# Kernel optimization log

Measured on AMD Instinct MI355X. Metric: run time of the kernel, lower is better.

Reference implementation:

```python
import jax, jax.numpy as jnp
import numpy as np

TOKENS = 16384
HIDDEN = 2048
GROUP_SIZE = 128
EPS = 1e-05
FP8_MAX = 448.0  # float8_e4m3fn max


def rmsnorm(x, w, eps=EPS):
    # vLLM RMSNorm: x * rsqrt(mean(x^2)) * weight
    var = jnp.mean(x * x, axis=-1, keepdims=True)
    return x * jax.lax.rsqrt(var + eps) * w


def fused_add_rmsnorm(x, residual, w, eps=EPS):
    # vLLM RMSNorm(x, residual): residual += x; out = rmsnorm(residual)
    resid = x + residual
    return rmsnorm(resid, w, eps), resid


def per_token_group_quant_fp8_ue8m0(y, group_size=GROUP_SIZE):
    # QuantFP8(static=False, group_shape=(1,128), use_ue8m0=True)
    t, h = y.shape
    g = y.reshape(t, h // group_size, group_size)
    amax = jnp.max(jnp.abs(g), axis=-1)                      # [T, H/G]
    scale = jnp.maximum(amax, 1e-10) / FP8_MAX
    scale = jnp.exp2(jnp.ceil(jnp.log2(scale)))              # ue8m0: round scale up to power of 2
    q = jnp.clip(g / scale[..., None], -FP8_MAX, FP8_MAX)
    q = q.astype(jnp.float8_e4m3fn)                          # fp8 rounding
    return q.reshape(t, h), scale


def setup_inputs() -> dict:
    key = jax.random.key(0)
    kx, kw = jax.random.split(key)
    x = jax.random.normal(kx, (TOKENS, HIDDEN), dtype=jnp.float32)
    norm_w = jnp.ones((4, HIDDEN), dtype=jnp.float32)
    w = jax.random.uniform(kw, (3, HIDDEN, HIDDEN), dtype=jnp.float32)
    return {"x": x, "norm_w": norm_w, "w": w}


def reference(x, norm_w, w):
    # tensor_model_parallel_all_reduce == identity at world_size 1
    z = jax.nn.relu(x)
    xr = z
    resid = z
    y = rmsnorm(xr, norm_w[0])
    x2 = y @ w[0]
    y2, resid = fused_add_rmsnorm(x2, resid, norm_w[1])
    y2_q, y2_s = per_token_group_quant_fp8_ue8m0(y2)
    x3 = y2_q.astype(x.dtype) @ w[1]
    y3, resid = fused_add_rmsnorm(x3, resid, norm_w[2])
    y3_q, y3_s = per_token_group_quant_fp8_ue8m0(y3)
    x4 = y3_q.astype(x.dtype) @ w[2]
    y4, resid = fused_add_rmsnorm(x4, resid, norm_w[3])
    return (y4, y2_s, y3_s)
```

## Files before the change

kernel.cpp:

```cpp
#include <hip/hip_runtime.h>
#include <stdint.h>
#include <math.h>

#define NTOK 16384
#define HID  2048
#define NGRP 16
#define EPSF 1e-5f

typedef __bf16 bf16;
typedef __bf16 bf16x8 __attribute__((ext_vector_type(8)));
typedef float  f32x4  __attribute__((ext_vector_type(4)));


__device__ __forceinline__ void async_load16(const void* g, void* l) {
  __builtin_amdgcn_global_load_lds((const __attribute__((address_space(1))) void*)g,
                                   (__attribute__((address_space(3))) void*)l, 16, 0, 0);
}

__device__ __forceinline__ float fp8_e4m3_rne(float v) {
  float a = fabsf(v);
  float s = (v < 0.f) ? -1.f : 1.f;
  if (a < 0.015625f) {
    float r = rintf(a * 512.0f);
    return s * r * 0.001953125f;
  }
  uint32_t u = __float_as_uint(a);
  u = (u + 0x7FFFFu + ((u >> 20) & 1u)) & 0xFFF00000u;
  return s * __uint_as_float(u);
}

__device__ __forceinline__ float block_sum256(float v) {
  __shared__ float sh[4];
  #pragma unroll
  for (int o = 32; o > 0; o >>= 1) v += __shfl_xor(v, o, 64);
  if ((threadIdx.x & 63) == 0) sh[threadIdx.x >> 6] = v;
  __syncthreads();
  return sh[0] + sh[1] + sh[2] + sh[3];
}

__device__ __forceinline__ float ue8m0_scale(float amax) {
  float v = fmaxf(amax, 1e-10f) / 448.0f;
  float l = (float)log2((double)v);
  return exp2f(ceilf(l));
}


__global__ __launch_bounds__(256) void k_transpose_cast(const float* __restrict__ W,
                                                        bf16* __restrict__ Wt) {
  __shared__ float tile[64][65];
  const size_t mat = (size_t)HID * HID;
  const float* Wz = W + mat * blockIdx.z;
  bf16* Wtz = Wt + mat * blockIdx.z;
  int bn = blockIdx.x * 64;
  int bk = blockIdx.y * 64;
  int t = threadIdx.x;
  {
    int r = t >> 4, c = (t & 15) * 4;
    #pragma unroll
    for (int i = 0; i < 4; i++) {
      float4 v = *(const float4*)(Wz + (size_t)(bk + r + 16 * i) * HID + bn + c);
      tile[r + 16 * i][c] = v.x; tile[r + 16 * i][c + 1] = v.y;
      tile[r + 16 * i][c + 2] = v.z; tile[r + 16 * i][c + 3] = v.w;
    }
  }
  __syncthreads();
  {
    int n = t >> 2, kc = (t & 3) * 16;
    bf16x8 o0, o1;
    #pragma unroll
    for (int j = 0; j < 8; j++) o0[j] = (bf16)tile[kc + j][n];
    #pragma unroll
    for (int j = 0; j < 8; j++) o1[j] = (bf16)tile[kc + 8 + j][n];
    bf16* dst = Wtz + (size_t)(bn + n) * HID + bk + kc;
    *(bf16x8*)dst = o0;
    *(bf16x8*)(dst + 8) = o1;
  }
}

__global__ __launch_bounds__(256) void k_pre(const float* __restrict__ x,
                                             const float* __restrict__ nw,
                                             bf16* __restrict__ Y,
                                             bf16* __restrict__ R) {
  size_t base = (size_t)blockIdx.x * HID + threadIdx.x * 8;
  float4 v0 = *(const float4*)(x + base);
  float4 v1 = *(const float4*)(x + base + 4);
  float z[8] = {v0.x, v0.y, v0.z, v0.w, v1.x, v1.y, v1.z, v1.w};
  float ss = 0.f;
  #pragma unroll
  for (int i = 0; i < 8; i++) { z[i] = fmaxf(z[i], 0.f); ss += z[i] * z[i]; }
  float tot = block_sum256(ss);
  float s = rsqrtf(tot * (1.0f / HID) + EPSF);
  bf16x8 rr;
  #pragma unroll
  for (int i = 0; i < 8; i++) rr[i] = (bf16)z[i];
  *(bf16x8*)(R + base) = rr;
  int j0 = threadIdx.x * 8;
  float4 w0 = *(const float4*)(nw + j0);
  float4 w1 = *(const float4*)(nw + j0 + 4);
  float wv[8] = {w0.x, w0.y, w0.z, w0.w, w1.x, w1.y, w1.z, w1.w};
  bf16x8 o;
  #pragma unroll
  for (int i = 0; i < 8; i++) o[i] = (bf16)(z[i] * s * wv[i]);
  *(bf16x8*)(Y + base) = o;
}

__global__ __launch_bounds__(256) void k_fuse_quant(const bf16* __restrict__ residIn,
                                                    const bf16* __restrict__ Cin,
                                                    const float* __restrict__ nw,
                                                    bf16* __restrict__ residOut,
                                                    bf16* __restrict__ Aout,
                                                    float* __restrict__ scaleOut) {
  int row = blockIdx.x;
  int j0 = threadIdx.x * 8;
  size_t base = (size_t)row * HID + j0;
  bf16x8 c  = *(const bf16x8*)(Cin + base);
  bf16x8 rv = *(const bf16x8*)(residIn + base);
  float r[8]; float ss = 0.f;
  #pragma unroll
  for (int i = 0; i < 8; i++) { r[i] = (float)rv[i] + (float)c[i]; ss += r[i] * r[i]; }
  float tot = block_sum256(ss);
  float s = rsqrtf(tot * (1.0f / HID) + EPSF);

  bf16x8 ro;
  #pragma unroll
  for (int i = 0; i < 8; i++) ro[i] = (bf16)r[i];
  *(bf16x8*)(residOut + base) = ro;

  float4 w0 = *(const float4*)(nw + j0);
  float4 w1 = *(const float4*)(nw + j0 + 4);
  float wv[8] = {w0.x, w0.y, w0.z, w0.w, w1.x, w1.y, w1.z, w1.w};
  float y[8], amax = 0.f;
  #pragma unroll
  for (int i = 0; i < 8; i++) { y[i] = r[i] * s * wv[i]; amax = fmaxf(amax, fabsf(y[i])); }
  amax = fmaxf(amax, __shfl_xor(amax, 1, 64));
  amax = fmaxf(amax, __shfl_xor(amax, 2, 64));
  amax = fmaxf(amax, __shfl_xor(amax, 4, 64));
  amax = fmaxf(amax, __shfl_xor(amax, 8, 64));
  float scale = ue8m0_scale(amax);
  float inv = 1.0f / scale;
  bf16x8 q;
  #pragma unroll
  for (int i = 0; i < 8; i++) {
    float t = fminf(fmaxf(y[i] * inv, -448.f), 448.f);
    q[i] = (bf16)fp8_e4m3_rne(t);
  }
  *(bf16x8*)(Aout + base) = q;
  if ((threadIdx.x & 15) == 0) scaleOut[(size_t)row * NGRP + (j0 >> 7)] = scale;
}

__global__ __launch_bounds__(256) void k_final(const bf16* __restrict__ residIn,
                                               const bf16* __restrict__ Cin,
                                               const float* __restrict__ nw,
                                               float* __restrict__ out) {
  size_t base = (size_t)blockIdx.x * HID + threadIdx.x * 8;
  bf16x8 c  = *(const bf16x8*)(Cin + base);
  bf16x8 rv = *(const bf16x8*)(residIn + base);
  float r[8]; float ss = 0.f;
  #pragma unroll
  for (int i = 0; i < 8; i++) { r[i] = (float)rv[i] + (float)c[i]; ss += r[i] * r[i]; }
  float tot = block_sum256(ss);
  float s = rsqrtf(tot * (1.0f / HID) + EPSF);
  int j0 = threadIdx.x * 8;
  float4 w0 = *(const float4*)(nw + j0);
  float4 w1 = *(const float4*)(nw + j0 + 4);
  float wv[8] = {w0.x, w0.y, w0.z, w0.w, w1.x, w1.y, w1.z, w1.w};
  float4 o0, o1;
  o0.x = r[0]*s*wv[0]; o0.y = r[1]*s*wv[1]; o0.z = r[2]*s*wv[2]; o0.w = r[3]*s*wv[3];
  o1.x = r[4]*s*wv[4]; o1.y = r[5]*s*wv[5]; o1.z = r[6]*s*wv[6]; o1.w = r[7]*s*wv[7];
  *(float4*)(out + base) = o0;
  *(float4*)(out + base + 4) = o1;
}

__global__ __launch_bounds__(512, 2) void k_gemm(const bf16* __restrict__ A,
                                                 const bf16* __restrict__ B,
                                                 bf16* __restrict__ C,
                                                 int M, int N, int K) {
  __shared__ __align__(16) char lds[2 * 65536];
  int b = blockIdx.x;
  int x = b & 7, j = b >> 3;
  int bm = x * 8 + (j & 7);
  int bn = j >> 3;
  int tid = threadIdx.x;
  int wave = tid >> 6, lane = tid & 63;
  int q = lane >> 4, rr = lane & 15;
  int wm = wave >> 2, wn = wave & 3;

  const bf16* aS[2][2]; const bf16* bS[2][2];
  #pragma unroll
  for (int ic = 0; ic < 2; ic++) {
    int m = ic * 512 + tid;
    int lr = m >> 3, cl = m & 7, lc = cl ^ (lr & 7);
    #pragma unroll
    for (int h = 0; h < 2; h++) {
      aS[h][ic] = A + (size_t)(bm * 256 + h * 128 + lr) * K + lc * 8;
      bS[h][ic] = B + (size_t)(bn * 256 + h * 128 + lr) * K + lc * 8;
    }
  }

  const int NT = K / 64;
  const int pc0 = (q ^ (rr & 7)) << 4;

#define STAGE_A(h, tt) {                                                       \
    int ts_ = (tt) < NT ? (tt) : (NT - 1);                                     \
    char* d_ = lds + (((tt) & 1) * 65536) + (h) * 16384 + tid * 16;            \
    async_load16(aS[h][0] + (size_t)ts_ * 64, d_);                             \
    async_load16(aS[h][1] + (size_t)ts_ * 64, d_ + 8192); }
#define STAGE_B(h, tt) {                                                       \
    int ts_ = (tt) < NT ? (tt) : (NT - 1);                                     \
    char* d_ = lds + (((tt) & 1) * 65536) + 32768 + (h) * 16384 + tid * 16;    \
    async_load16(bS[h][0] + (size_t)ts_ * 64, d_);                             \
    async_load16(bS[h][1] + (size_t)ts_ * 64, d_ + 8192); }

  f32x4 acc[8][4];
  #pragma unroll
  for (int mf = 0; mf < 8; mf++)
    #pragma unroll
    for (int nf = 0; nf < 4; nf++)
      #pragma unroll
      for (int e = 0; e < 4; e++) acc[mf][nf][e] = 0.f;

  STAGE_A(0, 0) STAGE_A(1, 0) STAGE_B(0, 0) STAGE_B(1, 0)
  STAGE_B(0, 1) STAGE_B(1, 1)
  asm volatile("s_waitcnt vmcnt(4)" ::: "memory");
  asm volatile("s_barrier" ::: "memory");

#define MFMA8(AF, BF, MO, NO)                                                  \
    __builtin_amdgcn_s_setprio(1);                                             \
    _Pragma("unroll")                                                          \
    for (int s = 0; s < 2; s++)                                                \
      _Pragma("unroll")                                                        \
      for (int f = 0; f < 4; f++)                                              \
        _Pragma("unroll")                                                      \
        for (int n2 = 0; n2 < 2; n2++)                                         \
          acc[(MO) + f][(NO) + n2] = __builtin_amdgcn_mfma_f32_16x16x32_bf16(  \
              AF[f][s], BF[n2][s], acc[(MO) + f][(NO) + n2], 0, 0, 0);         \
    __builtin_amdgcn_s_setprio(0);

#define TILE(tau, XB) {                                                        \
    const char* Ax_ = lds + (XB) + wm * 16384;                                 \
    const char* Bx_ = lds + (XB) + 32768 + wn * 8192;                          \
    bf16x8 a0_[4][2], a1_[4][2], b0_[2][2], b1_[2][2];                         \
        \
    _Pragma("unroll")                                                          \
    for (int f = 0; f < 4; f++)                                                \
      _Pragma("unroll")                                                        \
      for (int s = 0; s < 2; s++)                                              \
        a0_[f][s] = *(const bf16x8*)(Ax_ + f * 2048 + rr * 128 +               \
                                     (pc0 ^ (s << 6)));                        \
    _Pragma("unroll")                                                          \
    for (int n2 = 0; n2 < 2; n2++)                                             \
      _Pragma("unroll")                                                        \
      for (int s = 0; s < 2; s++)                                              \
        b0_[n2][s] = *(const bf16x8*)(Bx_ + n2 * 2048 + rr * 128 +             \
                                      (pc0 ^ (s << 6)));                       \
    STAGE_A(0, (tau) + 1)                                                      \
    asm volatile("s_barrier" ::: "memory");                                    \
    MFMA8(a0_, b0_, 0, 0)                                                      \
                \
    _Pragma("unroll")                                                          \
    for (int n2 = 0; n2 < 2; n2++)                                             \
      _Pragma("unroll")                                                        \
      for (int s = 0; s < 2; s++)                                              \
        b1_[n2][s] = *(const bf16x8*)(Bx_ + 4096 + n2 * 2048 + rr * 128 +      \
                                      (pc0 ^ (s << 6)));                       \
    STAGE_A(1, (tau) + 1)                                                      \
    asm volatile("s_barrier" ::: "memory");                                    \
    MFMA8(a0_, b1_, 0, 2)                                                      \
                \
    _Pragma("unroll")                                                          \
    for (int f = 0; f < 4; f++)                                                \
      _Pragma("unroll")                                                        \
      for (int s = 0; s < 2; s++)                                              \
        a1_[f][s] = *(const bf16x8*)(Ax_ + 8192 + f * 2048 + rr * 128 +        \
                                     (pc0 ^ (s << 6)));                        \
    STAGE_B(0, (tau) + 2)                                                      \
    asm volatile("s_barrier" ::: "memory");                                    \
    MFMA8(a1_, b0_, 4, 0)                                                      \
       \
    STAGE_B(1, (tau) + 2)                                                      \
    asm volatile("s_waitcnt vmcnt(4)" ::: "memory");                           \
    asm volatile("s_barrier" ::: "memory");                                    \
    MFMA8(a1_, b1_, 4, 2)                                                      \
  }

  for (int tt = 0; tt < NT; tt += 2) {
    TILE(tt, 0)
    TILE(tt + 1, 65536)
  }
#undef TILE
#undef MFMA8
#undef STAGE_A
#undef STAGE_B

  asm volatile("s_waitcnt vmcnt(0)" ::: "memory");
  __syncthreads();
  {
    char* cb = lds;
    #pragma unroll
    for (int mf = 0; mf < 8; mf++)
      #pragma unroll
      for (int nf = 0; nf < 4; nf++)
        #pragma unroll
        for (int tt = 0; tt < 4; tt++) {
          int row = wm * 128 + mf * 16 + q * 4 + tt;
          int col = wn * 64 + nf * 16 + rr;
          *(bf16*)(cb + row * 512 + col * 2) = (bf16)acc[mf][nf][tt];
        }
  }
  __syncthreads();
  {
    const char* cb = lds;
    #pragma unroll
    for (int i = 0; i < 16; i++) {
      int chunk = i * 512 + tid;
      int row = chunk >> 5, cc = chunk & 31;
      bf16x8 v = *(const bf16x8*)(cb + chunk * 16);
      *(bf16x8*)(C + (size_t)(bm * 256 + row) * N + bn * 256 + cc * 8) = v;
    }
  }
}


extern "C" void kernel_launch(void* const* d_in, const int* in_sizes, int n_in,
                              void* d_out, int out_size, void* d_ws, size_t ws_size,
                              hipStream_t stream) {
  const float* x      = (const float*)d_in[0];
  const float* norm_w = (const float*)d_in[1];
  const float* w      = (const float*)d_in[2];

  float* out   = (float*)d_out;
  float* y4o   = out;
  float* s2o   = out + (size_t)NTOK * HID;
  float* s3o   = s2o + (size_t)NTOK * NGRP;

  char* ws = (char*)d_ws;
  const size_t WT_B = (size_t)3 * HID * HID * 2;
  const size_t AB_B = (size_t)NTOK * HID * 2;
  bf16* Wt   = (bf16*)ws;
  bf16* Abuf = (bf16*)(ws + WT_B);
  bf16* Cbuf = (bf16*)(ws + WT_B + AB_B);
  bf16* Rbuf = (bf16*)(ws + WT_B + 2 * AB_B);
  const size_t MATE = (size_t)HID * HID;

  dim3 gT(HID / 64, HID / 64, 3);
  int  gG = (NTOK / 256) * (HID / 256);

  k_transpose_cast<<<gT, 256, 0, stream>>>(w, Wt);
  k_pre<<<NTOK, 256, 0, stream>>>(x, norm_w, Abuf, Rbuf);
  k_gemm<<<gG, 512, 0, stream>>>(Abuf, Wt, Cbuf, NTOK, HID, HID);
  k_fuse_quant<<<NTOK, 256, 0, stream>>>(Rbuf, Cbuf, norm_w + HID, Rbuf, Abuf, s2o);
  k_gemm<<<gG, 512, 0, stream>>>(Abuf, Wt + MATE, Cbuf, NTOK, HID, HID);
  k_fuse_quant<<<NTOK, 256, 0, stream>>>(Rbuf, Cbuf, norm_w + 2 * HID, Rbuf, Abuf, s3o);
  k_gemm<<<gG, 512, 0, stream>>>(Abuf, Wt + 2 * MATE, Cbuf, NTOK, HID, HID);
  k_final<<<NTOK, 256, 0, stream>>>(Rbuf, Cbuf, norm_w + 3 * HID, y4o);
}
```

Before: 702.2 us.

## Prefetch next tile's LDS fragments across iterations and swizzle epilogue LDS writes

Moves the first A/B fragment LDS reads of each K-tile into the tail of the previous tile, using ping-pong register sets, so the first MFMA group does not wait on LDS reads. Also reorders fragment loads to come after the barrier, ahead of their MFMA groups. Separately, it XOR-swizzles the column index in the C-staging LDS buffer to reduce bank conflicts in the epilogue. This adds register pressure and depends on the next buffer being ready after the vmcnt wait and barrier.

After: 698.6 us. About the same (-0.5%).

```diff
diff --git a/kernel.cpp b/kernel.cpp
--- a/kernel.cpp
+++ b/kernel.cpp
@@ -224,6 +224,22 @@
   asm volatile("s_waitcnt vmcnt(4)" ::: "memory");
   asm volatile("s_barrier" ::: "memory");
 
+  bf16x8 aF[4][2], bF[2][2], aG[4][2], bG[2][2];
+  {
+    const char* Ax = lds + wm * 16384;
+    const char* Bx = lds + 32768 + wn * 8192;
+    #pragma unroll
+    for (int f = 0; f < 4; f++)
+      #pragma unroll
+      for (int s = 0; s < 2; s++)
+        aF[f][s] = *(const bf16x8*)(Ax + f * 2048 + rr * 128 + (pc0 ^ (s << 6)));
+    #pragma unroll
+    for (int n2 = 0; n2 < 2; n2++)
+      #pragma unroll
+      for (int s = 0; s < 2; s++)
+        bF[n2][s] = *(const bf16x8*)(Bx + n2 * 2048 + rr * 128 + (pc0 ^ (s << 6)));
+  }
+
 #define MFMA8(AF, BF, MO, NO)                                                  \
     __builtin_amdgcn_s_setprio(1);                                             \
     _Pragma("unroll")                                                          \
@@ -236,56 +252,58 @@
               AF[f][s], BF[n2][s], acc[(MO) + f][(NO) + n2], 0, 0, 0);         \
     __builtin_amdgcn_s_setprio(0);
 
-#define TILE(tau, XB) {                                                        \
-    const char* Ax_ = lds + (XB) + wm * 16384;                                 \
-    const char* Bx_ = lds + (XB) + 32768 + wn * 8192;                          \
-    bf16x8 a0_[4][2], a1_[4][2], b0_[2][2], b1_[2][2];                         \
-        \
-    _Pragma("unroll")                                                          \
-    for (int f = 0; f < 4; f++)                                                \
-      _Pragma("unroll")                                                        \
-      for (int s = 0; s < 2; s++)                                              \
-        a0_[f][s] = *(const bf16x8*)(Ax_ + f * 2048 + rr * 128 +               \
-                                     (pc0 ^ (s << 6)));                        \
-    _Pragma("unroll")                                                          \
-    for (int n2 = 0; n2 < 2; n2++)                                             \
-      _Pragma("unroll")                                                        \
-      for (int s = 0; s < 2; s++)                                              \
-        b0_[n2][s] = *(const bf16x8*)(Bx_ + n2 * 2048 + rr * 128 +             \
-                                      (pc0 ^ (s << 6)));                       \
+#define TILE(tau, XB, AC, BC, AN, BN) {                                        \
+    const char* Ax_  = lds + (XB) + wm * 16384;                                \
+    const char* Bx_  = lds + (XB) + 32768 + wn * 8192;                         \
+    const char* AxN_ = lds + ((XB) ^ 65536) + wm * 16384;                      \
+    const char* BxN_ = lds + ((XB) ^ 65536) + 32768 + wn * 8192;               \
+    bf16x8 a1_[4][2], b1_[2][2];                                               \
+     \
     STAGE_A(0, (tau) + 1)                                                      \
     asm volatile("s_barrier" ::: "memory");                                    \
-    MFMA8(a0_, b0_, 0, 0)                                                      \
-                \
     _Pragma("unroll")                                                          \
     for (int n2 = 0; n2 < 2; n2++)                                             \
       _Pragma("unroll")                                                        \
       for (int s = 0; s < 2; s++)                                              \
         b1_[n2][s] = *(const bf16x8*)(Bx_ + 4096 + n2 * 2048 + rr * 128 +      \
                                       (pc0 ^ (s << 6)));                       \
+    MFMA8(AC, BC, 0, 0)                                                        \
+       \
     STAGE_A(1, (tau) + 1)                                                      \
     asm volatile("s_barrier" ::: "memory");                                    \
-    MFMA8(a0_, b1_, 0, 2)                                                      \
-                \
     _Pragma("unroll")                                                          \
     for (int f = 0; f < 4; f++)                                                \
       _Pragma("unroll")                                                        \
       for (int s = 0; s < 2; s++)                                              \
         a1_[f][s] = *(const bf16x8*)(Ax_ + 8192 + f * 2048 + rr * 128 +        \
                                      (pc0 ^ (s << 6)));                        \
+    MFMA8(AC, b1_, 0, 2)                                                       \
+                         \
     STAGE_B(0, (tau) + 2)                                                      \
     asm volatile("s_barrier" ::: "memory");                                    \
-    MFMA8(a1_, b0_, 4, 0)                                                      \
-       \
+    MFMA8(a1_, BC, 4, 0)                                                       \
+                              \
     STAGE_B(1, (tau) + 2)                                                      \
     asm volatile("s_waitcnt vmcnt(4)" ::: "memory");                           \
     asm volatile("s_barrier" ::: "memory");                                    \
+    _Pragma("unroll")                                                          \
+    for (int f = 0; f < 4; f++)                                                \
+      _Pragma("unroll")                                                        \
+      for (int s = 0; s < 2; s++)                                              \
+        AN[f][s] = *(const bf16x8*)(AxN_ + f * 2048 + rr * 128 +               \
+                                    (pc0 ^ (s << 6)));                         \
+    _Pragma("unroll")                                                          \
+    for (int n2 = 0; n2 < 2; n2++)                                             \
+      _Pragma("unroll")                                                        \
+      for (int s = 0; s < 2; s++)                                              \
+        BN[n2][s] = *(const bf16x8*)(BxN_ + n2 * 2048 + rr * 128 +             \
+                                     (pc0 ^ (s << 6)));                        \
     MFMA8(a1_, b1_, 4, 2)                                                      \
   }
 
   for (int tt = 0; tt < NT; tt += 2) {
-    TILE(tt, 0)
-    TILE(tt + 1, 65536)
+    TILE(tt,     0,     aF, bF, aG, bG)
+    TILE(tt + 1, 65536, aG, bG, aF, bF)
   }
 #undef TILE
 #undef MFMA8
@@ -304,7 +322,8 @@
         for (int tt = 0; tt < 4; tt++) {
           int row = wm * 128 + mf * 16 + q * 4 + tt;
           int col = wn * 64 + nf * 16 + rr;
-          *(bf16*)(cb + row * 512 + col * 2) = (bf16)acc[mf][nf][tt];
+          int cs  = col ^ (((row >> 2) & 3) << 4);
+          *(bf16*)(cb + row * 512 + cs * 2) = (bf16)acc[mf][nf][tt];
         }
   }
   __syncthreads();
@@ -314,7 +333,8 @@
     for (int i = 0; i < 16; i++) {
       int chunk = i * 512 + tid;
       int row = chunk >> 5, cc = chunk & 31;
-      bf16x8 v = *(const bf16x8*)(cb + chunk * 16);
+      int cs  = cc ^ (((row >> 2) & 3) << 1);
+      bf16x8 v = *(const bf16x8*)(cb + (row * 32 + cs) * 16);
       *(bf16x8*)(C + (size_t)(bm * 256 + row) * N + bn * 256 + cc * 8) = v;
     }
   }
```
